# Performance work log

Hardware: AMD Instinct MI355X
Metric: run time of the kernel (lower is better)

The kernel has to match this reference:

```python
import jax, jax.numpy as jnp
import numpy as np

B, S, D, H = 2, 2048, 768, 12
HD = D // H


def setup_inputs() -> dict:
    key = jax.random.key(0)
    ks = jax.random.split(key, 6)
    sc = 1.0 / np.sqrt(D)
    return {
        "x": jax.random.normal(ks[0], (B, S, D), dtype=jnp.float32),
        "mask": jnp.tril(jnp.ones((S, S), dtype=jnp.int32)),  # causal GPT mask
        "Wq": jax.random.normal(ks[1], (D, D), dtype=jnp.float32) * sc,
        "bq": jnp.zeros((D,), dtype=jnp.float32),
        "Wk": jax.random.normal(ks[2], (D, D), dtype=jnp.float32) * sc,
        "bk": jnp.zeros((D,), dtype=jnp.float32),
        "Wv": jax.random.normal(ks[3], (D, D), dtype=jnp.float32) * sc,
        "bv": jnp.zeros((D,), dtype=jnp.float32),
        "Wo": jax.random.normal(ks[4], (D, D), dtype=jnp.float32) * sc,
        "bo": jnp.zeros((D,), dtype=jnp.float32),
    }


def reference(x, mask, Wq, bq, Wk, bk, Wv, bv, Wo, bo):
    # Linear projections (torch Linear: x @ W.T + b; here W stored as [in,out])
    Q = (x @ Wq + bq).reshape(B, S, H, HD).transpose(0, 2, 1, 3)  # [B,H,S,HD]
    K = (x @ Wk + bk).reshape(B, S, H, HD).transpose(0, 2, 1, 3)
    V = (x @ Wv + bv).reshape(B, S, H, HD).transpose(0, 2, 1, 3)

    scores = jnp.einsum('bhqd,bhkd->bhqk', Q, K) / jnp.sqrt(jnp.float32(HD))
    scores = jnp.where(mask[None, None, :, :] == 0, jnp.float32(-1e9), scores)
    attn_weights = jax.nn.softmax(scores, axis=-1)  # dropout is identity in eval
    attn_out = jnp.einsum('bhqk,bhkd->bhqd', attn_weights, V)

    attn_out = attn_out.transpose(0, 2, 1, 3).reshape(B, S, D)
    out = attn_out @ Wo + bo
    return out, attn_weights
```

## Files before the change

kernel.cpp:

```cpp
#include <hip/hip_runtime.h>

#define DEV static __device__ __forceinline__

typedef __bf16 bf16x8 __attribute__((ext_vector_type(8)));
typedef float  f32x4  __attribute__((ext_vector_type(4)));

DEV bf16x8 ld8(const __bf16* p) { return *reinterpret_cast<const bf16x8*>(p); }

DEV f32x4 mfma16(bf16x8 a, bf16x8 b, f32x4 c) {
  return __builtin_amdgcn_mfma_f32_16x16x32_bf16(a, b, c, 0, 0, 0);
}

#define SEQ 2048
#define DIM 768
#define NH  12
#define HDIM 64

DEV void decode_chunk2(int cid, int CH, int& qt, int& t0) {
  int q = 0, rem = cid;
  while (true) {
    int nc = (2 * q + 2 + CH - 1) / CH;
    if (rem < nc) break;
    rem -= nc; ++q;
  }
  qt = q; t0 = rem * CH;
}

__global__ __launch_bounds__(256) void cvt_x(const float* __restrict__ x,
                                             __bf16* __restrict__ xb) {
  const int i = (blockIdx.x * 256 + threadIdx.x) * 8;
  f32x4 a = *(const f32x4*)(x + i);
  f32x4 b = *(const f32x4*)(x + i + 4);
  bf16x8 v;
  #pragma unroll
  for (int j = 0; j < 4; ++j) { v[j] = (__bf16)a[j]; v[4 + j] = (__bf16)b[j]; }
  *(bf16x8*)(xb + i) = v;
}

__global__ __launch_bounds__(256) void prep_wt(
    const float* __restrict__ Wq, const float* __restrict__ Wk,
    const float* __restrict__ Wv, const float* __restrict__ Wo,
    __bf16* __restrict__ WbT) {
  __shared__ float T[64][65];
  const int z = blockIdx.z;
  const float* W = (z == 0) ? Wq : (z == 1) ? Wk : (z == 2) ? Wv : Wo;
  const int kb = blockIdx.x * 64, nb = blockIdx.y * 64;
  const int t = threadIdx.x, r = t >> 2, c4 = (t & 3) * 16;
  #pragma unroll
  for (int j = 0; j < 16; j += 4) {
    f32x4 v = *(const f32x4*)(W + (size_t)(kb + r) * DIM + nb + c4 + j);
    T[r][c4 + j]     = v[0]; T[r][c4 + j + 1] = v[1];
    T[r][c4 + j + 2] = v[2]; T[r][c4 + j + 3] = v[3];
  }
  __syncthreads();
  bf16x8 o0, o1;
  #pragma unroll
  for (int j = 0; j < 8; ++j) {
    o0[j] = (__bf16)T[c4 + j][r];
    o1[j] = (__bf16)T[c4 + 8 + j][r];
  }
  __bf16* dst = WbT + (size_t)z * DIM * DIM + (size_t)(nb + r) * DIM + kb + c4;
  *(bf16x8*)dst = o0;
  *(bf16x8*)(dst + 8) = o1;
}

DEV void gemm_tile(const float* __restrict__ Af, const __bf16* __restrict__ Ab,
                   const __bf16* __restrict__ Bt,
                   const float* __restrict__ bias, void* __restrict__ outp,
                   const int mode, const float scale,
                   const int mbase, const int nbase) {
  __shared__ __bf16 As[64][72];
  __shared__ __bf16 Bs[64][72];

  const int tid  = threadIdx.x;
  const int l    = tid & 63;
  const int w    = tid >> 6;
  const int lrow = l & 15;
  const int lk8  = (l >> 4) * 8;
  const int wrow = (w >> 1) * 32, wcol = (w & 1) * 32;

  f32x4 acc[2][2] = {};

  const int arow = tid >> 2;
  const int acol = (tid & 3) * 16;

  for (int kk = 0; kk < DIM; kk += 64) {
    if (Ab) {
      const __bf16* asrc = Ab + (size_t)(mbase + arow) * DIM + kk + acol;
      *(bf16x8*)&As[arow][acol]     = ld8(asrc);
      *(bf16x8*)&As[arow][acol + 8] = ld8(asrc + 8);
    } else {
      const float* src = Af + (size_t)(mbase + arow) * DIM + kk + acol;
      f32x4 f0 = *(const f32x4*)(src);
      f32x4 f1 = *(const f32x4*)(src + 4);
      f32x4 f2 = *(const f32x4*)(src + 8);
      f32x4 f3 = *(const f32x4*)(src + 12);
      bf16x8 v0, v1;
      #pragma unroll
      for (int j = 0; j < 4; ++j) {
        v0[j] = (__bf16)f0[j]; v0[4 + j] = (__bf16)f1[j];
        v1[j] = (__bf16)f2[j]; v1[4 + j] = (__bf16)f3[j];
      }
      *(bf16x8*)&As[arow][acol]     = v0;
      *(bf16x8*)&As[arow][acol + 8] = v1;
    }
    {
      const __bf16* bsrc = Bt + (size_t)(nbase + arow) * DIM + kk + acol;
      *(bf16x8*)&Bs[arow][acol]     = ld8(bsrc);
      *(bf16x8*)&Bs[arow][acol + 8] = ld8(bsrc + 8);
    }
    __syncthreads();
    #pragma unroll
    for (int kc = 0; kc < 2; ++kc) {
      bf16x8 a0 = ld8(&As[wrow + lrow][kc * 32 + lk8]);
      bf16x8 a1 = ld8(&As[wrow + 16 + lrow][kc * 32 + lk8]);
      bf16x8 b0 = ld8(&Bs[wcol + lrow][kc * 32 + lk8]);
      bf16x8 b1 = ld8(&Bs[wcol + 16 + lrow][kc * 32 + lk8]);
      acc[0][0] = mfma16(a0, b0, acc[0][0]);
      acc[0][1] = mfma16(a0, b1, acc[0][1]);
      acc[1][0] = mfma16(a1, b0, acc[1][0]);
      acc[1][1] = mfma16(a1, b1, acc[1][1]);
    }
    __syncthreads();
  }

  #pragma unroll
  for (int mi = 0; mi < 2; ++mi)
  #pragma unroll
  for (int ni = 0; ni < 2; ++ni) {
    const int n  = nbase + wcol + ni * 16 + lrow;
    const float bn = bias[n];
    const int hh = n >> 6, hd = n & 63;
    #pragma unroll
    for (int r = 0; r < 4; ++r) {
      const int m = mbase + wrow + mi * 16 + (l >> 4) * 4 + r;
      const float v = (acc[mi][ni][r] + bn) * scale;
      const int bb = m >> 11, s = m & (SEQ - 1);
      if (mode == 0) {
        ((__bf16*)outp)[(((size_t)(bb * NH + hh) * SEQ) + s) * HDIM + hd] = (__bf16)v;
      } else if (mode == 1) {
        ((__bf16*)outp)[(((size_t)(bb * NH + hh) * HDIM) + hd) * SEQ + s] = (__bf16)v;
      } else {
        ((float*)outp)[(size_t)m * DIM + n] = v;
      }
    }
  }
}

__global__ __launch_bounds__(256, 4) void qkv_gemm(
    const __bf16* __restrict__ xb, const __bf16* __restrict__ WbT,
    const float* __restrict__ bq, const float* __restrict__ bk,
    const float* __restrict__ bv,
    __bf16* __restrict__ Qb, __bf16* __restrict__ Kb, __bf16* __restrict__ Vt) {
  const int z = blockIdx.z;
  const __bf16* Bt = WbT + (size_t)z * DIM * DIM;
  const float* bs = (z == 0) ? bq : (z == 1) ? bk : bv;
  void* o = (z == 0) ? (void*)Qb : (z == 1) ? (void*)Kb : (void*)Vt;
  const float sc = (z == 0) ? 0.125f : 1.f;
  gemm_tile(nullptr, xb, Bt, bs, o, (z == 2) ? 1 : 0, sc,
            blockIdx.y * 64, blockIdx.x * 64);
}

__global__ __launch_bounds__(256, 4) void out_gemm(
    const float* __restrict__ A, const __bf16* __restrict__ WbT,
    const float* __restrict__ bo, float* __restrict__ out) {
  gemm_tile(A, nullptr, WbT + (size_t)3 * DIM * DIM, bo, out, 2, 1.f,
            blockIdx.y * 64, blockIdx.x * 64);
}

__global__ __launch_bounds__(256) void zero_f32(float* __restrict__ p, int n4) {
  const f32x4 zv = {0.f, 0.f, 0.f, 0.f};
  int i = blockIdx.x * 256 + threadIdx.x;
  const int stride = gridDim.x * 256;
  for (; i < n4; i += stride) ((f32x4*)p)[i] = zv;
}

__global__ __launch_bounds__(256, 4) void attn_sums(
    const __bf16* __restrict__ Q, const __bf16* __restrict__ K,
    float* __restrict__ sums, float* __restrict__ Wout) {
  const int tid = threadIdx.x, l = tid & 63, w = tid >> 6;
  const int lrow = l & 15, lk8 = (l >> 4) * 8, g = l >> 4;
  const int lin = blockIdx.x;
  const int C = 72;
  const int bh = (lin & 7) * 3 + (lin >> 3) / C;
  const int cid = (lin >> 3) % C;
  int qt, t0; decode_chunk2(cid, 4, qt, t0);
  const int tmax = 2 * qt + 2;
  const int t1 = (t0 + 4 < tmax) ? t0 + 4 : tmax;
  const int fb0 = qt * 128 + w * 32;
  const int fb1 = fb0 + 16;
  const int q0 = fb0 + lrow, q1 = fb1 + lrow;

  const __bf16* Qh = Q + (size_t)bh * SEQ * HDIM;
  const __bf16* Kh = K + (size_t)bh * SEQ * HDIM;
  const bf16x8 bqA0 = ld8(Qh + (size_t)q0 * HDIM + lk8);
  const bf16x8 bqA1 = ld8(Qh + (size_t)q0 * HDIM + 32 + lk8);
  const bf16x8 bqB0 = ld8(Qh + (size_t)q1 * HDIM + lk8);
  const bf16x8 bqB1 = ld8(Qh + (size_t)q1 * HDIM + 32 + lk8);

  float sA = 0.f, sB = 0.f;
  for (int t = t0; t < t1; ++t) {
    const int kb = t * 64;
    const bool liveA = (kb <= fb0 + 15);
    const bool liveB = (kb <= fb1 + 15);
    if (!liveB) continue;
    #pragma unroll
    for (int nt = 0; nt < 4; ++nt) {
      const int krow = kb + nt * 16 + lrow;
      const bf16x8 ak0 = ld8(Kh + (size_t)krow * HDIM + lk8);
      const bf16x8 ak1 = ld8(Kh + (size_t)krow * HDIM + 32 + lk8);
      const int k0 = kb + nt * 16 + g * 4;
      if (liveA) {
        f32x4 s0 = {0.f, 0.f, 0.f, 0.f}, s1 = {0.f, 0.f, 0.f, 0.f};
        s0 = mfma16(ak0, bqA0, s0);
        s1 = mfma16(ak1, bqA1, s1);
        if (kb + 63 <= fb0) {
          #pragma unroll
          for (int r = 0; r < 4; ++r) sA += __expf(s0[r] + s1[r]);
        } else {
          #pragma unroll
          for (int r = 0; r < 4; ++r)
            sA += (k0 + r <= q0) ? __expf(s0[r] + s1[r]) : 0.f;
        }
      }
      {
        f32x4 s0 = {0.f, 0.f, 0.f, 0.f}, s1 = {0.f, 0.f, 0.f, 0.f};
        s0 = mfma16(ak0, bqB0, s0);
        s1 = mfma16(ak1, bqB1, s1);
        if (kb + 63 <= fb1) {
          #pragma unroll
          for (int r = 0; r < 4; ++r) sB += __expf(s0[r] + s1[r]);
        } else {
          #pragma unroll
          for (int r = 0; r < 4; ++r)
            sB += (k0 + r <= q1) ? __expf(s0[r] + s1[r]) : 0.f;
        }
      }
    }
  }
  sA += __shfl_xor(sA, 16); sA += __shfl_xor(sA, 32);
  sB += __shfl_xor(sB, 16); sB += __shfl_xor(sB, 32);
  if (g == 0) {
    unsafeAtomicAdd(&sums[bh * SEQ + q0], sA);
    unsafeAtomicAdd(&sums[bh * SEQ + q1], sB);
  }

  const int tz = (t1 < 2 * qt) ? t1 : 2 * qt;
  if (t0 < tz) {
    float* Wg = Wout + (size_t)bh * SEQ * SEQ;
    const int zr = tid >> 2;
    const int zc = (tid & 3) * 32;
    const f32x4 zv = {0.f, 0.f, 0.f, 0.f};
    for (int t = t0; t < tz; ++t) {
      float* base = Wg + (size_t)(t * 64 + zr) * SEQ + qt * 128 + zc;
      #pragma unroll
      for (int c = 0; c < 8; ++c) *(f32x4*)(base + c * 4) = zv;
    }
  }
}

__global__ __launch_bounds__(256, 4) void attn_wpv(
    const __bf16* __restrict__ Q, const __bf16* __restrict__ K,
    const __bf16* __restrict__ VT, const float* __restrict__ sums,
    float* __restrict__ Wout, float* __restrict__ AOf) {
  __shared__ float Plds[4][2][16][68];

  const int tid = threadIdx.x, l = tid & 63, w = tid >> 6;
  const int lrow = l & 15, lk8 = (l >> 4) * 8, g = l >> 4;
  const int lin = blockIdx.x;
  const int C = 40;
  const int bh = (lin & 7) * 3 + (lin >> 3) / C;
  const int cid = (lin >> 3) % C;
  int qt, t0; decode_chunk2(cid, 8, qt, t0);
  const int tmax = 2 * qt + 2;
  const int t1 = (t0 + 8 < tmax) ? t0 + 8 : tmax;
  const int bb = bh / NH, hh = bh % NH;
  const int fb0 = qt * 128 + w * 32;
  const int fb1 = fb0 + 16;
  const int q0 = fb0 + lrow, q1 = fb1 + lrow;

  const __bf16* Qh = Q + (size_t)bh * SEQ * HDIM;
  const __bf16* Kh = K + (size_t)bh * SEQ * HDIM;
  const __bf16* Vh = VT + (size_t)bh * HDIM * SEQ;
  float* Wg = Wout + (size_t)bh * SEQ * SEQ;

  const bf16x8 bqA0 = ld8(Qh + (size_t)q0 * HDIM + lk8);
  const bf16x8 bqA1 = ld8(Qh + (size_t)q0 * HDIM + 32 + lk8);
  const bf16x8 bqB0 = ld8(Qh + (size_t)q1 * HDIM + lk8);
  const bf16x8 bqB1 = ld8(Qh + (size_t)q1 * HDIM + 32 + lk8);
  const float invA = 1.f / sums[bh * SEQ + q0];
  const float invB = 1.f / sums[bh * SEQ + q1];

  f32x4 accA[4] = {}, accB[4] = {};
  for (int t = t0; t < t1; ++t) {
    const int kb = t * 64;
    const bool liveA = (kb <= fb0 + 15);
    const bool liveB = (kb <= fb1 + 15);
    const f32x4 zv = {0.f, 0.f, 0.f, 0.f};
    if (!liveB) {
      #pragma unroll
      for (int nt = 0; nt < 4; ++nt) {
        const int k0 = kb + nt * 16 + g * 4;
        *(f32x4*)&Wg[(size_t)q0 * SEQ + k0] = zv;
        *(f32x4*)&Wg[(size_t)q1 * SEQ + k0] = zv;
      }
      continue;
    }
    #pragma unroll
    for (int nt = 0; nt < 4; ++nt) {
      const int krow = kb + nt * 16 + lrow;
      const bf16x8 ak0 = ld8(Kh + (size_t)krow * HDIM + lk8);
      const bf16x8 ak1 = ld8(Kh + (size_t)krow * HDIM + 32 + lk8);
      const int k0 = kb + nt * 16 + g * 4;
      f32x4 pvA = zv;
      if (liveA) {
        f32x4 s0 = {0.f, 0.f, 0.f, 0.f}, s1 = {0.f, 0.f, 0.f, 0.f};
        s0 = mfma16(ak0, bqA0, s0);
        s1 = mfma16(ak1, bqA1, s1);
        if (kb + 63 <= fb0) {
          #pragma unroll
          for (int r = 0; r < 4; ++r) pvA[r] = __expf(s0[r] + s1[r]) * invA;
        } else {
          #pragma unroll
          for (int r = 0; r < 4; ++r)
            pvA[r] = (k0 + r <= q0) ? __expf(s0[r] + s1[r]) * invA : 0.f;
        }
        *(f32x4*)&Plds[w][0][lrow][nt * 16 + g * 4] = pvA;
      }
      *(f32x4*)&Wg[(size_t)q0 * SEQ + k0] = pvA;
      f32x4 pvB;
      {
        f32x4 s0 = {0.f, 0.f, 0.f, 0.f}, s1 = {0.f, 0.f, 0.f, 0.f};
        s0 = mfma16(ak0, bqB0, s0);
        s1 = mfma16(ak1, bqB1, s1);
        if (kb + 63 <= fb1) {
          #pragma unroll
          for (int r = 0; r < 4; ++r) pvB[r] = __expf(s0[r] + s1[r]) * invB;
        } else {
          #pragma unroll
          for (int r = 0; r < 4; ++r)
            pvB[r] = (k0 + r <= q1) ? __expf(s0[r] + s1[r]) * invB : 0.f;
        }
      }
      *(f32x4*)&Wg[(size_t)q1 * SEQ + k0] = pvB;
      *(f32x4*)&Plds[w][1][lrow][nt * 16 + g * 4] = pvB;
    }
    #pragma unroll
    for (int kc = 0; kc < 2; ++kc) {
      bf16x8 awA, awB;
      if (liveA) {
        const float* ps = &Plds[w][0][lrow][kc * 32 + lk8];
        const f32x4 p0 = *(const f32x4*)ps;
        const f32x4 p1 = *(const f32x4*)(ps + 4);
        #pragma unroll
        for (int j = 0; j < 4; ++j) { awA[j] = (__bf16)p0[j]; awA[4 + j] = (__bf16)p1[j]; }
      }
      {
        const float* ps = &Plds[w][1][lrow][kc * 32 + lk8];
        const f32x4 p0 = *(const f32x4*)ps;
        const f32x4 p1 = *(const f32x4*)(ps + 4);
        #pragma unroll
        for (int j = 0; j < 4; ++j) { awB[j] = (__bf16)p0[j]; awB[4 + j] = (__bf16)p1[j]; }
      }
      #pragma unroll
      for (int nt = 0; nt < 4; ++nt) {
        const bf16x8 bv =
            ld8(Vh + (size_t)(nt * 16 + lrow) * SEQ + kb + kc * 32 + lk8);
        if (liveA) accA[nt] = mfma16(awA, bv, accA[nt]);
        accB[nt] = mfma16(awB, bv, accB[nt]);
      }
    }
  }

  #pragma unroll
  for (int nt = 0; nt < 4; ++nt)
    #pragma unroll
    for (int r = 0; r < 4; ++r) {
      unsafeAtomicAdd(
          &AOf[(size_t)(bb * SEQ + fb0 + g * 4 + r) * DIM + hh * HDIM + nt * 16 + lrow],
          accA[nt][r]);
      unsafeAtomicAdd(
          &AOf[(size_t)(bb * SEQ + fb1 + g * 4 + r) * DIM + hh * HDIM + nt * 16 + lrow],
          accB[nt][r]);
    }
}

extern "C" void kernel_launch(void* const* d_in, const int* in_sizes, int n_in,
                              void* d_out, int out_size, void* d_ws, size_t ws_size,
                              hipStream_t stream) {
  const float* x  = (const float*)d_in[0];
  const float* Wq = (const float*)d_in[2];
  const float* bq = (const float*)d_in[3];
  const float* Wk = (const float*)d_in[4];
  const float* bk = (const float*)d_in[5];
  const float* Wv = (const float*)d_in[6];
  const float* bv = (const float*)d_in[7];
  const float* Wo = (const float*)d_in[8];
  const float* bo = (const float*)d_in[9];

  char* wsb = (char*)d_ws;
  __bf16* Qb   = (__bf16*)(wsb);
  __bf16* Kb   = (__bf16*)(wsb + 6291456);
  __bf16* Vt   = (__bf16*)(wsb + 12582912);
  float*  AOf  = (float*)(wsb + 18874368);
  float*  sums = (float*)(wsb + 31457280);
  __bf16* WbT  = (__bf16*)(wsb + 31653888);

  float* out   = (float*)d_out;
  float* attnW = out + 3145728;
  __bf16* xb   = (__bf16*)attnW;

  zero_f32<<<1024, 256, 0, stream>>>(AOf, (3145728 + 49152) / 4);
  cvt_x<<<1536, 256, 0, stream>>>(x, xb);
  prep_wt<<<dim3(12, 12, 4), 256, 0, stream>>>(Wq, Wk, Wv, Wo, WbT);
  qkv_gemm<<<dim3(12, 64, 3), 256, 0, stream>>>(xb, WbT, bq, bk, bv, Qb, Kb, Vt);
  attn_sums<<<1728, 256, 0, stream>>>(Qb, Kb, sums, attnW);
  attn_wpv<<<960, 256, 0, stream>>>(Qb, Kb, Vt, sums, attnW, AOf);
  out_gemm<<<dim3(12, 64), 256, 0, stream>>>(AOf, WbT, bo, out);
}
```

Measured before the change: 279.8 us.

## Enlarge GEMM tiles to 128x128 and merge zero/convert prep kernels

The QKV and output projection GEMMs move from 64x64 to 128x128 block tiles, with each wave computing a 64x64 sub-tile (4x4 MFMA accumulators). This cuts global-load and sync overhead per FLOP, at the cost of fewer blocks (576 QKV, 192 out) and more registers. Launch bounds drop to 2 blocks per SM to match. The zero-fill and x-to-bf16 conversion kernels are fused into one launch to save a kernel launch. The new unpadded 64-wide LDS rows may cause bank conflicts.

```diff
diff --git a/kernel.cpp b/kernel.cpp
--- a/kernel.cpp
+++ b/kernel.cpp
@@ -26,15 +26,23 @@
   qt = q; t0 = rem * CH;
 }
 
-__global__ __launch_bounds__(256) void cvt_x(const float* __restrict__ x,
-                                             __bf16* __restrict__ xb) {
-  const int i = (blockIdx.x * 256 + threadIdx.x) * 8;
-  f32x4 a = *(const f32x4*)(x + i);
-  f32x4 b = *(const f32x4*)(x + i + 4);
-  bf16x8 v;
-  #pragma unroll
-  for (int j = 0; j < 4; ++j) { v[j] = (__bf16)a[j]; v[4 + j] = (__bf16)b[j]; }
-  *(bf16x8*)(xb + i) = v;
+__global__ __launch_bounds__(256) void prep_misc(const float* __restrict__ x,
+                                                 __bf16* __restrict__ xb,
+                                                 float* __restrict__ zp) {
+  const int bid = blockIdx.x, tid = threadIdx.x;
+  if (bid < 1024) {
+    const int n4 = (3145728 + 49152) / 4;
+    const f32x4 zv = {0.f, 0.f, 0.f, 0.f};
+    for (int i = bid * 256 + tid; i < n4; i += 1024 * 256) ((f32x4*)zp)[i] = zv;
+  } else {
+    const int i = ((bid - 1024) * 256 + tid) * 8;
+    f32x4 a = *(const f32x4*)(x + i);
+    f32x4 b = *(const f32x4*)(x + i + 4);
+    bf16x8 v;
+    #pragma unroll
+    for (int j = 0; j < 4; ++j) { v[j] = (__bf16)a[j]; v[4 + j] = (__bf16)b[j]; }
+    *(bf16x8*)(xb + i) = v;
+  }
 }
 
 __global__ __launch_bounds__(256) void prep_wt(
@@ -64,76 +72,81 @@
   *(bf16x8*)(dst + 8) = o1;
 }
 
-DEV void gemm_tile(const float* __restrict__ Af, const __bf16* __restrict__ Ab,
-                   const __bf16* __restrict__ Bt,
-                   const float* __restrict__ bias, void* __restrict__ outp,
-                   const int mode, const float scale,
-                   const int mbase, const int nbase) {
-  __shared__ __bf16 As[64][72];
-  __shared__ __bf16 Bs[64][72];
+DEV void gemm128(const float* __restrict__ Af, const __bf16* __restrict__ Ab,
+                 const __bf16* __restrict__ Bt,
+                 const float* __restrict__ bias, void* __restrict__ outp,
+                 const int mode, const float scale,
+                 const int mbase, const int nbase) {
+  __shared__ __bf16 As[128][64];
+  __shared__ __bf16 Bs[128][64];
 
   const int tid  = threadIdx.x;
   const int l    = tid & 63;
   const int w    = tid >> 6;
   const int lrow = l & 15;
   const int lk8  = (l >> 4) * 8;
-  const int wrow = (w >> 1) * 32, wcol = (w & 1) * 32;
-
-  f32x4 acc[2][2] = {};
-
-  const int arow = tid >> 2;
-  const int acol = (tid & 3) * 16;
+  const int wr = (w >> 1) * 64, wc = (w & 1) * 64;
+
+  f32x4 acc[4][4] = {};
+
+  const int srow = tid >> 1;
+  const int scol = (tid & 1) * 32;
 
   for (int kk = 0; kk < DIM; kk += 64) {
     if (Ab) {
-      const __bf16* asrc = Ab + (size_t)(mbase + arow) * DIM + kk + acol;
-      *(bf16x8*)&As[arow][acol]     = ld8(asrc);
-      *(bf16x8*)&As[arow][acol + 8] = ld8(asrc + 8);
+      const __bf16* a = Ab + (size_t)(mbase + srow) * DIM + kk + scol;
+      *(bf16x8*)&As[srow][scol]      = ld8(a);
+      *(bf16x8*)&As[srow][scol + 8]  = ld8(a + 8);
+      *(bf16x8*)&As[srow][scol + 16] = ld8(a + 16);
+      *(bf16x8*)&As[srow][scol + 24] = ld8(a + 24);
     } else {
-      const float* src = Af + (size_t)(mbase + arow) * DIM + kk + acol;
-      f32x4 f0 = *(const f32x4*)(src);
-      f32x4 f1 = *(const f32x4*)(src + 4);
-      f32x4 f2 = *(const f32x4*)(src + 8);
-      f32x4 f3 = *(const f32x4*)(src + 12);
-      bf16x8 v0, v1;
-      #pragma unroll
-      for (int j = 0; j < 4; ++j) {
-        v0[j] = (__bf16)f0[j]; v0[4 + j] = (__bf16)f1[j];
-        v1[j] = (__bf16)f2[j]; v1[4 + j] = (__bf16)f3[j];
-      }
-      *(bf16x8*)&As[arow][acol]     = v0;
-      *(bf16x8*)&As[arow][acol + 8] = v1;
+      const float* a = Af + (size_t)(mbase + srow) * DIM + kk + scol;
+      #pragma unroll
+      for (int h = 0; h < 4; ++h) {
+        f32x4 f0 = *(const f32x4*)(a + h * 8);
+        f32x4 f1 = *(const f32x4*)(a + h * 8 + 4);
+        bf16x8 v;
+        #pragma unroll
+        for (int j = 0; j < 4; ++j) { v[j] = (__bf16)f0[j]; v[4 + j] = (__bf16)f1[j]; }
+        *(bf16x8*)&As[srow][scol + h * 8] = v;
+      }
     }
     {
-      const __bf16* bsrc = Bt + (size_t)(nbase + arow) * DIM + kk + acol;
-      *(bf16x8*)&Bs[arow][acol]     = ld8(bsrc);
-      *(bf16x8*)&Bs[arow][acol + 8] = ld8(bsrc + 8);
+      const __bf16* b = Bt + (size_t)(nbase + srow) * DIM + kk + scol;
+      *(bf16x8*)&Bs[srow][scol]      = ld8(b);
+      *(bf16x8*)&Bs[srow][scol + 8]  = ld8(b + 8);
+      *(bf16x8*)&Bs[srow][scol + 16] = ld8(b + 16);
+      *(bf16x8*)&Bs[srow][scol + 24] = ld8(b + 24);
     }
     __syncthreads();
     #pragma unroll
     for (int kc = 0; kc < 2; ++kc) {
-      bf16x8 a0 = ld8(&As[wrow + lrow][kc * 32 + lk8]);
-      bf16x8 a1 = ld8(&As[wrow + 16 + lrow][kc * 32 + lk8]);
-      bf16x8 b0 = ld8(&Bs[wcol + lrow][kc * 32 + lk8]);
-      bf16x8 b1 = ld8(&Bs[wcol + 16 + lrow][kc * 32 + lk8]);
-      acc[0][0] = mfma16(a0, b0, acc[0][0]);
-      acc[0][1] = mfma16(a0, b1, acc[0][1]);
-      acc[1][0] = mfma16(a1, b0, acc[1][0]);
-      acc[1][1] = mfma16(a1, b1, acc[1][1]);
+      bf16x8 af[4], bf[4];
+      #pragma unroll
+      for (int mi = 0; mi < 4; ++mi)
+        af[mi] = ld8(&As[wr + mi * 16 + lrow][kc * 32 + lk8]);
+      #pragma unroll
+      for (int ni = 0; ni < 4; ++ni)
+        bf[ni] = ld8(&Bs[wc + ni * 16 + lrow][kc * 32 + lk8]);
+      #pragma unroll
+      for (int mi = 0; mi < 4; ++mi)
+        #pragma unroll
+        for (int ni = 0; ni < 4; ++ni)
+          acc[mi][ni] = mfma16(af[mi], bf[ni], acc[mi][ni]);
     }
     __syncthreads();
   }
 
   #pragma unroll
-  for (int mi = 0; mi < 2; ++mi)
+  for (int mi = 0; mi < 4; ++mi)
   #pragma unroll
-  for (int ni = 0; ni < 2; ++ni) {
-    const int n  = nbase + wcol + ni * 16 + lrow;
+  for (int ni = 0; ni < 4; ++ni) {
+    const int n  = nbase + wc + ni * 16 + lrow;
     const float bn = bias[n];
     const int hh = n >> 6, hd = n & 63;
     #pragma unroll
     for (int r = 0; r < 4; ++r) {
-      const int m = mbase + wrow + mi * 16 + (l >> 4) * 4 + r;
+      const int m = mbase + wr + mi * 16 + (l >> 4) * 4 + r;
       const float v = (acc[mi][ni][r] + bn) * scale;
       const int bb = m >> 11, s = m & (SEQ - 1);
       if (mode == 0) {
@@ -147,7 +160,7 @@
   }
 }
 
-__global__ __launch_bounds__(256, 4) void qkv_gemm(
+__global__ __launch_bounds__(256, 2) void qkv_gemm(
     const __bf16* __restrict__ xb, const __bf16* __restrict__ WbT,
     const float* __restrict__ bq, const float* __restrict__ bk,
     const float* __restrict__ bv,
@@ -157,22 +170,15 @@
   const float* bs = (z == 0) ? bq : (z == 1) ? bk : bv;
   void* o = (z == 0) ? (void*)Qb : (z == 1) ? (void*)Kb : (void*)Vt;
   const float sc = (z == 0) ? 0.125f : 1.f;
-  gemm_tile(nullptr, xb, Bt, bs, o, (z == 2) ? 1 : 0, sc,
-            blockIdx.y * 64, blockIdx.x * 64);
-}
-
-__global__ __launch_bounds__(256, 4) void out_gemm(
+  gemm128(nullptr, xb, Bt, bs, o, (z == 2) ? 1 : 0, sc,
+          blockIdx.y * 128, blockIdx.x * 128);
+}
+
+__global__ __launch_bounds__(256, 2) void out_gemm(
     const float* __restrict__ A, const __bf16* __restrict__ WbT,
     const float* __restrict__ bo, float* __restrict__ out) {
-  gemm_tile(A, nullptr, WbT + (size_t)3 * DIM * DIM, bo, out, 2, 1.f,
-            blockIdx.y * 64, blockIdx.x * 64);
-}
-
-__global__ __launch_bounds__(256) void zero_f32(float* __restrict__ p, int n4) {
-  const f32x4 zv = {0.f, 0.f, 0.f, 0.f};
-  int i = blockIdx.x * 256 + threadIdx.x;
-  const int stride = gridDim.x * 256;
-  for (; i < n4; i += stride) ((f32x4*)p)[i] = zv;
+  gemm128(A, nullptr, WbT + (size_t)3 * DIM * DIM, bo, out, 2, 1.f,
+          blockIdx.y * 128, blockIdx.x * 128);
 }
 
 __global__ __launch_bounds__(256, 4) void attn_sums(
@@ -410,11 +416,10 @@
   float* attnW = out + 3145728;
   __bf16* xb   = (__bf16*)attnW;
 
-  zero_f32<<<1024, 256, 0, stream>>>(AOf, (3145728 + 49152) / 4);
-  cvt_x<<<1536, 256, 0, stream>>>(x, xb);
+  prep_misc<<<2560, 256, 0, stream>>>(x, xb, AOf);
   prep_wt<<<dim3(12, 12, 4), 256, 0, stream>>>(Wq, Wk, Wv, Wo, WbT);
-  qkv_gemm<<<dim3(12, 64, 3), 256, 0, stream>>>(xb, WbT, bq, bk, bv, Qb, Kb, Vt);
+  qkv_gemm<<<dim3(6, 32, 3), 256, 0, stream>>>(xb, WbT, bq, bk, bv, Qb, Kb, Vt);
   attn_sums<<<1728, 256, 0, stream>>>(Qb, Kb, sums, attnW);
   attn_wpv<<<960, 256, 0, stream>>>(Qb, Kb, Vt, sums, attnW, AOf);
-  out_gemm<<<dim3(12, 64), 256, 0, stream>>>(AOf, WbT, bo, out);
-}
+  out_gemm<<<dim3(6, 32), 256, 0, stream>>>(AOf, WbT, bo, out);
+}
```

New measurement: 304.1 us. 8.7% more time.
